# Kernel optimization log

Hardware: AMD Instinct MI355X
Metric: run time of the kernel (lower is better)

Reference implementation:

```python
import jax, jax.numpy as jnp
import numpy as np

B, D, O = 16384, 1024, 2048
MU, LAM = 0.9, 0.1


def setup_inputs() -> dict:
    key = jax.random.key(0)
    ks = jax.random.split(key, 16)
    stdv = float(1.0 / np.sqrt(D))
    u = lambda k, shape, s: jax.random.uniform(k, shape, jnp.float32, -s, s)
    return {
        "x": jax.random.normal(ks[0], (B, D), jnp.float32),
        "x_ctx": jax.random.normal(ks[1], (B, D), jnp.float32),
        "classifier": u(ks[2], (O, D), stdv),
        "none_tensor": u(ks[3], (1, D), stdv),
        "ctx_q_w": u(ks[4], (O, D), stdv),
        "ctx_q_b": u(ks[5], (O,), stdv),
        "word_g_w": u(ks[6], (1, D), stdv),
        "word_g_b": u(ks[7], (1,), stdv),
        "tcq_w1": u(ks[8], (D, D), stdv),
        "tcq_b1": u(ks[9], (D,), stdv),
        "tcq_w2": u(ks[10], (O, D), stdv),
        "tcq_b2": u(ks[11], (O,), stdv),
        "history_input": 0.1 * jax.random.normal(ks[12], (O - 1, D), jnp.float32),
        "history_count": jax.random.randint(ks[13], (O - 1,), 0, 10),
        "labels": jax.random.randint(ks[14], (B,), 0, O),
    }


def reference(x, x_ctx, classifier, none_tensor, ctx_q_w, ctx_q_b,
              word_g_w, word_g_b, tcq_w1, tcq_b1, tcq_w2, tcq_b2,
              history_input, history_count, labels):
    mu, lam = MU, LAM
    # ---- update_history (torch.no_grad), vectorized over classes via segment_sum ----
    xs = jax.lax.stop_gradient(x)
    sums = jax.ops.segment_sum(xs, labels, num_segments=O)               # [O, D]
    counts = jax.ops.segment_sum(jnp.ones((B,), jnp.float32), labels, num_segments=O)  # [O]
    has = counts[1:] > 0                                                  # classes 1..O-1
    cls_mean = sums[1:] / jnp.maximum(counts[1:], 1.0)[:, None]
    hist = jnp.where(has[:, None], mu * history_input + cls_mean, history_input)
    cnt = history_count + has.astype(history_count.dtype)
    # ---- generate_substitute (mu < 1 branch) ----
    denom = 1.0 - jnp.power(mu, jnp.maximum(cnt, 1).astype(jnp.float32))[:, None]
    v = hist * (1.0 - mu) / denom                                        # [O-1, D]
    r_sub = jnp.concatenate([none_tensor, v], axis=0)                    # [O, D]
    ctx_logits = x_ctx @ ctx_q_w.T + ctx_q_b                              # [B, O]
    att_logits = jax.nn.gelu(x @ tcq_w1.T + tcq_b1, approximate=False) @ tcq_w2.T + tcq_b2  # [B, O]
    # ---- gated combine + bilinear classifier (training=True path: w uses ctx_logits) ----
    g_word = jax.nn.sigmoid(x @ word_g_w.T + word_g_b)                    # [B, 1]
    w = g_word * jax.nn.sigmoid(ctx_logits)                               # [B, O]
    # logits = sum(((1-w)*x[:,None,:] + w*r_sub) * classifier, -1), collapsed algebraically
    logits = (1.0 - w) * (x @ classifier.T) + w * jnp.einsum('od,od->o', r_sub, classifier)[None, :]
    # ---- losses on labels >= 0 (mask-weighted means, jit-safe) ----
    mask = (labels >= 0).astype(jnp.float32)
    n = jnp.maximum(mask.sum(), 1.0)
    lsm = jax.nn.log_softmax(logits, axis=-1)
    nll = -jnp.take_along_axis(lsm, jnp.maximum(labels, 0)[:, None], axis=1)[:, 0]
    ce = (mask * nll).sum() / n
    mse_row = jnp.mean((ctx_logits - att_logits) ** 2, axis=-1)
    mse = (mask * mse_row).sum() / n
    return (ce + lam * mse, logits)
```

## Files before the change

kernel.cpp:

```cpp
#include <hip/hip_runtime.h>
#include <cstdint>
#include <cstddef>

#define DEV __device__ __forceinline__

typedef __attribute__((ext_vector_type(4))) float f32x4;
typedef __attribute__((ext_vector_type(8))) short bf16x8;
typedef unsigned short ushort_t;
typedef __attribute__((ext_vector_type(8))) unsigned short ushort8;

static constexpr int B_ = 16384, D_ = 1024, O_ = 2048;
static constexpr float LAM_ = 0.1f;

static constexpr size_t WS_XBF   = 0;
static constexpr size_t WS_XCBF  = WS_XBF   + (size_t)B_ * D_ * 2;
static constexpr size_t WS_HBF   = WS_XCBF  + (size_t)B_ * D_ * 2;
static constexpr size_t WS_CLSBF = WS_HBF   + (size_t)B_ * D_ * 2;
static constexpr size_t WS_CTWBF = WS_CLSBF + (size_t)O_ * D_ * 2;
static constexpr size_t WS_W2BF  = WS_CTWBF + (size_t)O_ * D_ * 2;
static constexpr size_t WS_W1BF  = WS_W2BF  + (size_t)O_ * D_ * 2;
static constexpr size_t WS_SMALL = WS_W1BF  + (size_t)D_ * D_ * 2;
static constexpr size_t SM_COUNTS = 0;
static constexpr size_t SM_TSUM   = 8192;
static constexpr size_t SM_MSE    = 16384;
static constexpr size_t SM_ZERO_BYTES = 82176;
static constexpr size_t SM_S      = 82176;
static constexpr size_t SM_GWORD  = 90368;
static constexpr size_t SM_CEROW  = 155904;

DEV float wave_sum(float v) {
  #pragma unroll
  for (int o = 32; o; o >>= 1) v += __shfl_xor(v, o, 64);
  return v;
}

DEV ushort_t f2bf1(float f) {
  union { float f; unsigned u; } c{f};
  unsigned r = c.u + 0x7fffu + ((c.u >> 16) & 1u);
  return (ushort_t)(r >> 16);
}

DEV float sigmoidf(float z) { return 1.0f / (1.0f + expf(-z)); }

DEV void gload_lds16(const ushort_t* g, ushort_t* l) {
  __builtin_amdgcn_global_load_lds((const __attribute__((address_space(1))) void*)g,
                                   (__attribute__((address_space(3))) void*)l, 16, 0, 0);
}

DEV void stage2(const ushort_t* __restrict__ s0, ushort_t* slot, int tid) {
  gload_lds16(s0, slot + tid * 8);
  gload_lds16(s0 + 128 * 1024, slot + (tid + 512) * 8);
}

DEV f32x4 mfma16(bf16x8 a, bf16x8 b, f32x4 c) {
  return __builtin_amdgcn_mfma_f32_16x16x32_bf16(a, b, c, 0, 0, 0);
}

#define DSR(dst, addr, off) \
  asm volatile("ds_read_b128 %0, %1 offset:" off : "=v"(dst) : "v"(addr))

template<int N> DEV void wait_vm() {
  if constexpr (N == 8)      asm volatile("s_waitcnt vmcnt(8)" ::: "memory");
  else if constexpr (N == 6) asm volatile("s_waitcnt vmcnt(6)" ::: "memory");
  else if constexpr (N == 4) asm volatile("s_waitcnt vmcnt(4)" ::: "memory");
  else if constexpr (N == 2) asm volatile("s_waitcnt vmcnt(2)" ::: "memory");
  else                       asm volatile("s_waitcnt vmcnt(0)" ::: "memory");
}

__global__ __launch_bounds__(256) void f2bf_kernel(const float* __restrict__ in,
                                                   ushort_t* __restrict__ out, int n8) {
  int i = blockIdx.x * 256 + threadIdx.x;
  if (i >= n8) return;
  const float4* p = (const float4*)(in + (size_t)i * 8);
  float4 a = p[0], b = p[1];
  ushort8 o;
  o[0] = f2bf1(a.x); o[1] = f2bf1(a.y); o[2] = f2bf1(a.z); o[3] = f2bf1(a.w);
  o[4] = f2bf1(b.x); o[5] = f2bf1(b.y); o[6] = f2bf1(b.z); o[7] = f2bf1(b.w);
  *(ushort8*)(out + (size_t)i * 8) = o;
}

__global__ __launch_bounds__(256) void rowdot_kernel(const float* __restrict__ x,
    const float* __restrict__ cls, const float* __restrict__ wg,
    const float* __restrict__ wgb, const int* __restrict__ labels,
    float* __restrict__ tsum, float* __restrict__ counts, float* __restrict__ g_word) {
  int wave = threadIdx.x >> 6, lane = threadIdx.x & 63;
  int row = blockIdx.x * 4 + wave;
  const float* xr = x + (size_t)row * D_;
  int lab = labels[row];
  const float* cr = cls + (size_t)max(lab, 0) * D_;
  float t = 0.f, g = 0.f;
  #pragma unroll
  for (int j = 0; j < 4; ++j) {
    int d = j * 256 + lane * 4;
    float4 xv = *(const float4*)(xr + d);
    float4 cv = *(const float4*)(cr + d);
    float4 wv = *(const float4*)(wg + d);
    t += xv.x * cv.x + xv.y * cv.y + xv.z * cv.z + xv.w * cv.w;
    g += xv.x * wv.x + xv.y * wv.y + xv.z * wv.z + xv.w * wv.w;
  }
  t = wave_sum(t); g = wave_sum(g);
  if (lane == 0) {
    if (lab >= 0) {
      atomicAdd(&tsum[lab], t);
      atomicAdd(&counts[lab], 1.0f);
    }
    g_word[row] = sigmoidf(g + wgb[0]);
  }
}

__global__ __launch_bounds__(256) void scls_kernel(const float* __restrict__ cls,
    const float* __restrict__ none_t, const float* __restrict__ hist,
    const int* __restrict__ hcnt, const float* __restrict__ counts,
    const float* __restrict__ tsum, float* __restrict__ s) {
  int wave = threadIdx.x >> 6, lane = threadIdx.x & 63;
  int o = blockIdx.x * 4 + wave;
  if (o >= O_) return;
  const float* cr = cls + (size_t)o * D_;
  const float* src = (o == 0) ? none_t : hist + (size_t)(o - 1) * D_;
  float dv = 0.f;
  #pragma unroll
  for (int j = 0; j < 4; ++j) {
    int d = j * 256 + lane * 4;
    float4 a = *(const float4*)(src + d);
    float4 c = *(const float4*)(cr + d);
    dv += a.x * c.x + a.y * c.y + a.z * c.z + a.w * c.w;
  }
  dv = wave_sum(dv);
  if (lane == 0) {
    if (o == 0) { s[0] = dv; }
    else {
      float co = counts[o];
      bool has = co > 0.f;
      int cnt = hcnt[o - 1] + (has ? 1 : 0);
      float denom = 1.f - powf(0.9f, (float)max(cnt, 1));
      float val = has ? (0.9f * dv + tsum[o] / fmaxf(co, 1.f)) : dv;
      s[o] = (0.1f / denom) * val;
    }
  }
}

template<bool S01, bool S23, int W0, int W1, int W2, int W3, bool RLAST>
DEV void tile4(int t, const ushort_t* __restrict__ sA0, const ushort_t* __restrict__ sB0,
               ushort_t* lds, int tid, unsigned aoffB, unsigned boffB,
               bf16x8 (&bA)[2][4], bf16x8 (&bB)[2][4], f32x4 (&acc)[8][4]) {
  const unsigned sl0 = (unsigned)(((2 * t) & 3) * 16384);
  const unsigned sl1 = (unsigned)(((2 * t + 1) & 3) * 16384);
  const unsigned sl2 = (unsigned)(((2 * t + 2) & 3) * 16384);
  const unsigned aA0 = aoffB + sl0;
  const unsigned aA1 = aoffB + sl1, aB1 = boffB + 65536u + sl1;
  const unsigned aA2 = aoffB + sl2, aB2 = boffB + 65536u + sl2;
  DSR(bA[1][0], aA0, "4096"); DSR(bA[1][1], aA0, "5120");
  DSR(bA[1][2], aA0, "6144"); DSR(bA[1][3], aA0, "7168");
  if constexpr (S01) stage2(sA0 + (size_t)(2 * t + 3) * 32, lds + ((2 * t + 3) & 3) * 8192, tid);
  asm volatile("s_waitcnt lgkmcnt(4)");
  __builtin_amdgcn_sched_barrier(0);
  __builtin_amdgcn_s_setprio(1);
  #pragma unroll
  for (int m = 0; m < 4; m++)
    #pragma unroll
    for (int n = 0; n < 4; n++) acc[m][n] = mfma16(bA[0][m], bB[0][n], acc[m][n]);
  __builtin_amdgcn_s_setprio(0);
  __builtin_amdgcn_sched_barrier(0);
  wait_vm<W0>();
  __builtin_amdgcn_s_barrier();
  DSR(bB[1][0], aB1, "0"); DSR(bB[1][1], aB1, "1024");
  DSR(bB[1][2], aB1, "2048"); DSR(bB[1][3], aB1, "3072");
  DSR(bA[0][0], aA1, "0"); DSR(bA[0][1], aA1, "1024");
  DSR(bA[0][2], aA1, "2048"); DSR(bA[0][3], aA1, "3072");
  if constexpr (S01) stage2(sB0 + (size_t)(2 * t + 3) * 32, lds + 32768 + ((2 * t + 3) & 3) * 8192, tid);
  asm volatile("s_waitcnt lgkmcnt(8)");
  __builtin_amdgcn_sched_barrier(0);
  __builtin_amdgcn_s_setprio(1);
  #pragma unroll
  for (int m = 0; m < 4; m++)
    #pragma unroll
    for (int n = 0; n < 4; n++) acc[m + 4][n] = mfma16(bA[1][m], bB[0][n], acc[m + 4][n]);
  __builtin_amdgcn_s_setprio(0);
  __builtin_amdgcn_sched_barrier(0);
  wait_vm<W1>();
  __builtin_amdgcn_s_barrier();
  DSR(bA[1][0], aA1, "4096"); DSR(bA[1][1], aA1, "5120");
  DSR(bA[1][2], aA1, "6144"); DSR(bA[1][3], aA1, "7168");
  if constexpr (S23) stage2(sA0 + (size_t)(2 * t + 4) * 32, lds + ((2 * t + 4) & 3) * 8192, tid);
  asm volatile("s_waitcnt lgkmcnt(4)");
  __builtin_amdgcn_sched_barrier(0);
  __builtin_amdgcn_s_setprio(1);
  #pragma unroll
  for (int m = 0; m < 4; m++)
    #pragma unroll
    for (int n = 0; n < 4; n++) acc[m][n] = mfma16(bA[0][m], bB[1][n], acc[m][n]);
  __builtin_amdgcn_s_setprio(0);
  __builtin_amdgcn_sched_barrier(0);
  wait_vm<W2>();
  __builtin_amdgcn_s_barrier();
  if constexpr (!RLAST) {
    DSR(bB[0][0], aB2, "0"); DSR(bB[0][1], aB2, "1024");
    DSR(bB[0][2], aB2, "2048"); DSR(bB[0][3], aB2, "3072");
    DSR(bA[0][0], aA2, "0"); DSR(bA[0][1], aA2, "1024");
    DSR(bA[0][2], aA2, "2048"); DSR(bA[0][3], aA2, "3072");
  }
  if constexpr (S23) stage2(sB0 + (size_t)(2 * t + 4) * 32, lds + 32768 + ((2 * t + 4) & 3) * 8192, tid);
  if constexpr (RLAST) asm volatile("s_waitcnt lgkmcnt(0)");
  else                 asm volatile("s_waitcnt lgkmcnt(8)");
  __builtin_amdgcn_sched_barrier(0);
  __builtin_amdgcn_s_setprio(1);
  #pragma unroll
  for (int m = 0; m < 4; m++)
    #pragma unroll
    for (int n = 0; n < 4; n++) acc[m + 4][n] = mfma16(bA[1][m], bB[1][n], acc[m + 4][n]);
  __builtin_amdgcn_s_setprio(0);
  __builtin_amdgcn_sched_barrier(0);
  wait_vm<W3>();
  __builtin_amdgcn_s_barrier();
}

template<int EPI, int NTSHIFT>
__global__ __launch_bounds__(512, 2) void gemm8_kernel(
    const ushort_t* __restrict__ A, const ushort_t* __restrict__ Bmat,
    const float* __restrict__ bias, float* __restrict__ fout,
    ushort_t* __restrict__ hout, const float* __restrict__ g_word,
    const float* __restrict__ svec, float* __restrict__ mse_row) {
  __shared__ __align__(16) ushort_t lds[65536];
  const int tid = threadIdx.x, lane = tid & 63, wave = tid >> 6;
  const int wr = wave >> 2, wc = wave & 3;
  const int nwg = 64 << NTSHIFT, cpx = nwg >> 3;
  int bid = blockIdx.x;
  int wg = (bid & 7) * cpx + (bid >> 3);
  const int bm = wg >> NTSHIFT, bn = wg & ((1 << NTSHIFT) - 1);
  const int NCOL = 256 << NTSHIFT;
  const int qsrc = (tid & 3) ^ ((tid >> 3) & 3);
  const ushort_t* sA0 = A + ((size_t)bm * 256 + (tid >> 2)) * 1024 + qsrc * 8;
  const ushort_t* sB0 = Bmat + ((size_t)bn * 256 + (tid >> 2)) * 1024 + qsrc * 8;
  const int qrd = (lane >> 4) ^ (((lane & 15) >> 1) & 3);
  const unsigned aoffB = (unsigned)(((wr * 128 + (lane & 15)) * 32 + qrd * 8) * 2);
  const unsigned boffB = (unsigned)(((wc * 64 + (lane & 15)) * 32 + qrd * 8) * 2);
  f32x4 acc[8][4] = {};
  stage2(sA0, lds, tid);
  stage2(sB0, lds + 32768, tid);
  stage2(sA0 + 32, lds + 8192, tid);
  stage2(sB0 + 32, lds + 32768 + 8192, tid);
  stage2(sA0 + 64, lds + 2 * 8192, tid);
  stage2(sB0 + 64, lds + 32768 + 2 * 8192, tid);
  asm volatile("s_waitcnt vmcnt(8)" ::: "memory");
  __builtin_amdgcn_s_barrier();
  bf16x8 bA[2][4], bB[2][4];
  {
    const unsigned aB0 = boffB + 65536u;
    DSR(bB[0][0], aB0, "0"); DSR(bB[0][1], aB0, "1024");
    DSR(bB[0][2], aB0, "2048"); DSR(bB[0][3], aB0, "3072");
    DSR(bA[0][0], aoffB, "0"); DSR(bA[0][1], aoffB, "1024");
    DSR(bA[0][2], aoffB, "2048"); DSR(bA[0][3], aoffB, "3072");
  }
  for (int t = 0; t < 14; ++t)
    tile4<true, true, 6, 6, 6, 6, false>(t, sA0, sB0, lds, tid, aoffB, boffB, bA, bB, acc);
  tile4<true, false, 6, 6, 4, 2, false>(14, sA0, sB0, lds, tid, aoffB, boffB, bA, bB, acc);
  tile4<false, false, 0, 0, 0, 0, true>(15, sA0, sB0, lds, tid, aoffB, boffB, bA, bB, acc);
  #pragma unroll
  for (int m = 0; m < 8; m++) {
    #pragma unroll
    for (int i = 0; i < 4; i++) {
      int row = bm * 256 + wr * 128 + m * 16 + (lane >> 4) * 4 + i;
      float gw = 0.f, msum = 0.f;
      if constexpr (EPI == 3) gw = g_word[row];
      #pragma unroll
      for (int n = 0; n < 4; n++) {
        int col = bn * 256 + wc * 64 + n * 16 + (lane & 15);
        float v = acc[m][n][i];
        if constexpr (EPI == 0) {
          float z = v + bias[col];
          float gl = 0.5f * z * (1.f + erff(z * 0.70710678118f));
          hout[(size_t)row * 1024 + col] = f2bf1(gl);
        } else if constexpr (EPI == 1) {
          fout[(size_t)row * NCOL + col] = v + bias[col];
        } else if constexpr (EPI == 2) {
          float att = v + bias[col];
          float ctx = fout[(size_t)row * NCOL + col];
          float d = ctx - att;
          msum += d * d;
        } else {
          size_t off = (size_t)row * NCOL + col;
          float ctx = fout[off];
          float w = gw * sigmoidf(ctx);
          fout[off] = (1.f - w) * v + w * svec[col];
        }
      }
      if constexpr (EPI == 2) {
        #pragma unroll
        for (int o = 1; o < 16; o <<= 1) msum += __shfl_xor(msum, o, 64);
        if ((lane & 15) == 0) atomicAdd(&mse_row[row], msum);
      }
    }
  }
}

__global__ __launch_bounds__(256) void ce_kernel(const float* __restrict__ logits,
    const int* __restrict__ labels, float* __restrict__ ce_row) {
  int row = blockIdx.x, t = threadIdx.x, lane = t & 63, wave = t >> 6;
  const float* lr = logits + (size_t)row * O_;
  float v[8];
  float m = -INFINITY;
  #pragma unroll
  for (int j = 0; j < 8; j++) { v[j] = lr[t + j * 256]; m = fmaxf(m, v[j]); }
  #pragma unroll
  for (int o = 32; o; o >>= 1) m = fmaxf(m, __shfl_xor(m, o, 64));
  __shared__ float red[8];
  if (lane == 0) red[wave] = m;
  __syncthreads();
  m = fmaxf(fmaxf(red[0], red[1]), fmaxf(red[2], red[3]));
  float se = 0.f;
  #pragma unroll
  for (int j = 0; j < 8; j++) se += expf(v[j] - m);
  se = wave_sum(se);
  if (lane == 0) red[4 + wave] = se;
  __syncthreads();
  if (t == 0) {
    float bs = red[4] + red[5] + red[6] + red[7];
    int lab = labels[row];
    float nll = 0.f;
    if (lab >= 0) nll = -(lr[lab] - m - logf(bs));
    ce_row[row] = nll;
  }
}

__global__ __launch_bounds__(256) void finalize_kernel(const float* __restrict__ ce_row,
    const float* __restrict__ mse_row, const int* __restrict__ labels,
    float* __restrict__ out0) {
  int t = threadIdx.x, lane = t & 63, wave = t >> 6;
  float sn = 0.f, sm = 0.f, sc = 0.f;
  for (int i = t; i < B_; i += 256) {
    if (labels[i] >= 0) { sn += ce_row[i]; sm += mse_row[i]; sc += 1.f; }
  }
  sn = wave_sum(sn); sm = wave_sum(sm); sc = wave_sum(sc);
  __shared__ float r0[4], r1[4], r2[4];
  if (lane == 0) { r0[wave] = sn; r1[wave] = sm; r2[wave] = sc; }
  __syncthreads();
  if (t == 0) {
    float a = r0[0] + r0[1] + r0[2] + r0[3];
    float b = r1[0] + r1[1] + r1[2] + r1[3];
    float c = r2[0] + r2[1] + r2[2] + r2[3];
    out0[0] = (a + LAM_ * (b / (float)O_)) / fmaxf(c, 1.f);
  }
}

extern "C" void kernel_launch(void* const* d_in, const int* in_sizes, int n_in,
                              void* d_out, int out_size, void* d_ws, size_t ws_size,
                              hipStream_t stream) {
  const float* x        = (const float*)d_in[0];
  const float* x_ctx    = (const float*)d_in[1];
  const float* cls      = (const float*)d_in[2];
  const float* none_t   = (const float*)d_in[3];
  const float* ctx_q_w  = (const float*)d_in[4];
  const float* ctx_q_b  = (const float*)d_in[5];
  const float* word_g_w = (const float*)d_in[6];
  const float* word_g_b = (const float*)d_in[7];
  const float* w1       = (const float*)d_in[8];
  const float* b1       = (const float*)d_in[9];
  const float* w2       = (const float*)d_in[10];
  const float* b2       = (const float*)d_in[11];
  const float* hist     = (const float*)d_in[12];
  const int*   hcnt     = (const int*)d_in[13];
  const int*   labels   = (const int*)d_in[14];

  float* out  = (float*)d_out;
  float* out1 = out + 1;
  char* ws = (char*)d_ws;

  ushort_t* xbf   = (ushort_t*)(ws + WS_XBF);
  ushort_t* xcbf  = (ushort_t*)(ws + WS_XCBF);
  ushort_t* hbf   = (ushort_t*)(ws + WS_HBF);
  ushort_t* clsbf = (ushort_t*)(ws + WS_CLSBF);
  ushort_t* ctwbf = (ushort_t*)(ws + WS_CTWBF);
  ushort_t* w2bf  = (ushort_t*)(ws + WS_W2BF);
  ushort_t* w1bf  = (ushort_t*)(ws + WS_W1BF);
  float* counts   = (float*)(ws + WS_SMALL + SM_COUNTS);
  float* tsum     = (float*)(ws + WS_SMALL + SM_TSUM);
  float* mse_row  = (float*)(ws + WS_SMALL + SM_MSE);
  float* s        = (float*)(ws + WS_SMALL + SM_S);
  float* g_word   = (float*)(ws + WS_SMALL + SM_GWORD);
  float* ce_row   = (float*)(ws + WS_SMALL + SM_CEROW);

  hipMemsetAsync(ws + WS_SMALL, 0, SM_ZERO_BYTES, stream);

  f2bf_kernel<<<8192, 256, 0, stream>>>(x, xbf, B_ * D_ / 8);
  f2bf_kernel<<<8192, 256, 0, stream>>>(x_ctx, xcbf, B_ * D_ / 8);
  f2bf_kernel<<<1024, 256, 0, stream>>>(cls, clsbf, O_ * D_ / 8);
  f2bf_kernel<<<1024, 256, 0, stream>>>(ctx_q_w, ctwbf, O_ * D_ / 8);
  f2bf_kernel<<<1024, 256, 0, stream>>>(w2, w2bf, O_ * D_ / 8);
  f2bf_kernel<<<512, 256, 0, stream>>>(w1, w1bf, D_ * D_ / 8);

  rowdot_kernel<<<B_ / 4, 256, 0, stream>>>(x, cls, word_g_w, word_g_b, labels,
                                            tsum, counts, g_word);
  scls_kernel<<<O_ / 4, 256, 0, stream>>>(cls, none_t, hist, hcnt, counts, tsum, s);

  gemm8_kernel<0, 2><<<64 * 4, 512, 0, stream>>>(xbf, w1bf, b1, nullptr, hbf,
                                                 nullptr, nullptr, nullptr);
  gemm8_kernel<1, 3><<<64 * 8, 512, 0, stream>>>(xcbf, ctwbf, ctx_q_b, out1, nullptr,
                                                 nullptr, nullptr, nullptr);
  gemm8_kernel<2, 3><<<64 * 8, 512, 0, stream>>>(hbf, w2bf, b2, out1, nullptr,
                                                 nullptr, nullptr, mse_row);
  gemm8_kernel<3, 3><<<64 * 8, 512, 0, stream>>>(xbf, clsbf, nullptr, out1, nullptr,
                                                 g_word, s, nullptr);

  ce_kernel<<<B_, 256, 0, stream>>>(out1, labels, ce_row);
  finalize_kernel<<<1, 256, 0, stream>>>(ce_row, mse_row, labels, out);
}
```

Measured before the change: 455.0 us.

## Add alternative GEMM main-loop schedules for the second and classifier GEMMs

Adds two alternative K-loop schedules for the bf16 GEMM kernel, selected by a new template parameter. One alternates half-tile LDS reads and MFMA bursts with extra barriers and full lgkmcnt waits. The other loads all eight A fragments per k-step and issues 32 MFMAs per phase. The tcq_w2 GEMM now uses the first and the classifier GEMM uses the second, in place of the software-pipelined double-buffered register schedule. This lowers register pressure and simplifies ordering, but it drops the overlap of LDS reads with MFMA and adds more barriers.

Result: no change. 461.9 us (+1.5%).

```diff
diff --git a/kernel.cpp b/kernel.cpp
--- a/kernel.cpp
+++ b/kernel.cpp
@@ -139,8 +139,9 @@
   }
 }
 
+
 template<bool S01, bool S23, int W0, int W1, int W2, int W3, bool RLAST>
-DEV void tile4(int t, const ushort_t* __restrict__ sA0, const ushort_t* __restrict__ sB0,
+DEV void tileA(int t, const ushort_t* __restrict__ sA0, const ushort_t* __restrict__ sB0,
                ushort_t* lds, int tid, unsigned aoffB, unsigned boffB,
                bf16x8 (&bA)[2][4], bf16x8 (&bB)[2][4], f32x4 (&acc)[8][4]) {
   const unsigned sl0 = (unsigned)(((2 * t) & 3) * 16384);
@@ -214,7 +215,115 @@
   __builtin_amdgcn_s_barrier();
 }
 
-template<int EPI, int NTSHIFT>
+template<bool S01, bool S23, int W1, int W3>
+DEV void tileB(int t, const ushort_t* __restrict__ sA0, const ushort_t* __restrict__ sB0,
+               ushort_t* lds, int tid, unsigned aoffB, unsigned boffB, f32x4 (&acc)[8][4]) {
+  const unsigned sl0 = (unsigned)(((2 * t) & 3) * 16384);
+  const unsigned sl1 = (unsigned)(((2 * t + 1) & 3) * 16384);
+  const unsigned aA0 = aoffB + sl0, aB0 = boffB + 65536u + sl0;
+  const unsigned aA1 = aoffB + sl1, aB1 = boffB + 65536u + sl1;
+  bf16x8 fA[4], fB[4];
+  DSR(fB[0], aB0, "0"); DSR(fB[1], aB0, "1024"); DSR(fB[2], aB0, "2048"); DSR(fB[3], aB0, "3072");
+  DSR(fA[0], aA0, "0"); DSR(fA[1], aA0, "1024"); DSR(fA[2], aA0, "2048"); DSR(fA[3], aA0, "3072");
+  if constexpr (S01) stage2(sA0 + (size_t)(2 * t + 3) * 32, lds + ((2 * t + 3) & 3) * 8192, tid);
+  __builtin_amdgcn_s_barrier();
+  asm volatile("s_waitcnt lgkmcnt(0)");
+  __builtin_amdgcn_sched_barrier(0);
+  __builtin_amdgcn_s_setprio(1);
+  #pragma unroll
+  for (int m = 0; m < 4; m++)
+    #pragma unroll
+    for (int n = 0; n < 4; n++) acc[m][n] = mfma16(fA[m], fB[n], acc[m][n]);
+  __builtin_amdgcn_s_setprio(0);
+  __builtin_amdgcn_s_barrier();
+  DSR(fA[0], aA0, "4096"); DSR(fA[1], aA0, "5120"); DSR(fA[2], aA0, "6144"); DSR(fA[3], aA0, "7168");
+  if constexpr (S01) stage2(sB0 + (size_t)(2 * t + 3) * 32, lds + 32768 + ((2 * t + 3) & 3) * 8192, tid);
+  __builtin_amdgcn_s_barrier();
+  asm volatile("s_waitcnt lgkmcnt(0)");
+  __builtin_amdgcn_sched_barrier(0);
+  __builtin_amdgcn_s_setprio(1);
+  #pragma unroll
+  for (int m = 0; m < 4; m++)
+    #pragma unroll
+    for (int n = 0; n < 4; n++) acc[m + 4][n] = mfma16(fA[m], fB[n], acc[m + 4][n]);
+  __builtin_amdgcn_s_setprio(0);
+  wait_vm<W1>();
+  __builtin_amdgcn_s_barrier();
+  DSR(fB[0], aB1, "0"); DSR(fB[1], aB1, "1024"); DSR(fB[2], aB1, "2048"); DSR(fB[3], aB1, "3072");
+  DSR(fA[0], aA1, "0"); DSR(fA[1], aA1, "1024"); DSR(fA[2], aA1, "2048"); DSR(fA[3], aA1, "3072");
+  if constexpr (S23) stage2(sA0 + (size_t)(2 * t + 4) * 32, lds + ((2 * t + 4) & 3) * 8192, tid);
+  __builtin_amdgcn_s_barrier();
+  asm volatile("s_waitcnt lgkmcnt(0)");
+  __builtin_amdgcn_sched_barrier(0);
+  __builtin_amdgcn_s_setprio(1);
+  #pragma unroll
+  for (int m = 0; m < 4; m++)
+    #pragma unroll
+    for (int n = 0; n < 4; n++) acc[m][n] = mfma16(fA[m], fB[n], acc[m][n]);
+  __builtin_amdgcn_s_setprio(0);
+  __builtin_amdgcn_s_barrier();
+  DSR(fA[0], aA1, "4096"); DSR(fA[1], aA1, "5120"); DSR(fA[2], aA1, "6144"); DSR(fA[3], aA1, "7168");
+  if constexpr (S23) stage2(sB0 + (size_t)(2 * t + 4) * 32, lds + 32768 + ((2 * t + 4) & 3) * 8192, tid);
+  __builtin_amdgcn_s_barrier();
+  asm volatile("s_waitcnt lgkmcnt(0)");
+  __builtin_amdgcn_sched_barrier(0);
+  __builtin_amdgcn_s_setprio(1);
+  #pragma unroll
+  for (int m = 0; m < 4; m++)
+    #pragma unroll
+    for (int n = 0; n < 4; n++) acc[m + 4][n] = mfma16(fA[m], fB[n], acc[m + 4][n]);
+  __builtin_amdgcn_s_setprio(0);
+  wait_vm<W3>();
+  __builtin_amdgcn_s_barrier();
+}
+
+template<bool S01, bool S23, int WA, int WB>
+DEV void tileC(int t, const ushort_t* __restrict__ sA0, const ushort_t* __restrict__ sB0,
+               ushort_t* lds, int tid, unsigned aoffB, unsigned boffB, f32x4 (&acc)[8][4]) {
+  const unsigned sl0 = (unsigned)(((2 * t) & 3) * 16384);
+  const unsigned sl1 = (unsigned)(((2 * t + 1) & 3) * 16384);
+  const unsigned aA0 = aoffB + sl0, aB0 = boffB + 65536u + sl0;
+  const unsigned aA1 = aoffB + sl1, aB1 = boffB + 65536u + sl1;
+  bf16x8 fA[8], fB[4];
+  DSR(fB[0], aB0, "0"); DSR(fB[1], aB0, "1024"); DSR(fB[2], aB0, "2048"); DSR(fB[3], aB0, "3072");
+  DSR(fA[0], aA0, "0"); DSR(fA[1], aA0, "1024"); DSR(fA[2], aA0, "2048"); DSR(fA[3], aA0, "3072");
+  DSR(fA[4], aA0, "4096"); DSR(fA[5], aA0, "5120"); DSR(fA[6], aA0, "6144"); DSR(fA[7], aA0, "7168");
+  if constexpr (S01) {
+    stage2(sA0 + (size_t)(2 * t + 3) * 32, lds + ((2 * t + 3) & 3) * 8192, tid);
+    stage2(sB0 + (size_t)(2 * t + 3) * 32, lds + 32768 + ((2 * t + 3) & 3) * 8192, tid);
+  }
+  __builtin_amdgcn_s_barrier();
+  asm volatile("s_waitcnt lgkmcnt(0)");
+  __builtin_amdgcn_sched_barrier(0);
+  __builtin_amdgcn_s_setprio(1);
+  #pragma unroll
+  for (int m = 0; m < 8; m++)
+    #pragma unroll
+    for (int n = 0; n < 4; n++) acc[m][n] = mfma16(fA[m], fB[n], acc[m][n]);
+  __builtin_amdgcn_s_setprio(0);
+  wait_vm<WA>();
+  __builtin_amdgcn_s_barrier();
+  DSR(fB[0], aB1, "0"); DSR(fB[1], aB1, "1024"); DSR(fB[2], aB1, "2048"); DSR(fB[3], aB1, "3072");
+  DSR(fA[0], aA1, "0"); DSR(fA[1], aA1, "1024"); DSR(fA[2], aA1, "2048"); DSR(fA[3], aA1, "3072");
+  DSR(fA[4], aA1, "4096"); DSR(fA[5], aA1, "5120"); DSR(fA[6], aA1, "6144"); DSR(fA[7], aA1, "7168");
+  if constexpr (S23) {
+    stage2(sA0 + (size_t)(2 * t + 4) * 32, lds + ((2 * t + 4) & 3) * 8192, tid);
+    stage2(sB0 + (size_t)(2 * t + 4) * 32, lds + 32768 + ((2 * t + 4) & 3) * 8192, tid);
+  }
+  __builtin_amdgcn_s_barrier();
+  asm volatile("s_waitcnt lgkmcnt(0)");
+  __builtin_amdgcn_sched_barrier(0);
+  __builtin_amdgcn_s_setprio(1);
+  #pragma unroll
+  for (int m = 0; m < 8; m++)
+    #pragma unroll
+    for (int n = 0; n < 4; n++) acc[m][n] = mfma16(fA[m], fB[n], acc[m][n]);
+  __builtin_amdgcn_s_setprio(0);
+  wait_vm<WB>();
+  __builtin_amdgcn_s_barrier();
+}
+
+template<int EPI, int NTSHIFT, int SCHED>
 __global__ __launch_bounds__(512, 2) void gemm8_kernel(
     const ushort_t* __restrict__ A, const ushort_t* __restrict__ Bmat,
     const float* __restrict__ bias, float* __restrict__ fout,
@@ -243,18 +352,30 @@
   stage2(sB0 + 64, lds + 32768 + 2 * 8192, tid);
   asm volatile("s_waitcnt vmcnt(8)" ::: "memory");
   __builtin_amdgcn_s_barrier();
-  bf16x8 bA[2][4], bB[2][4];
-  {
-    const unsigned aB0 = boffB + 65536u;
-    DSR(bB[0][0], aB0, "0"); DSR(bB[0][1], aB0, "1024");
-    DSR(bB[0][2], aB0, "2048"); DSR(bB[0][3], aB0, "3072");
-    DSR(bA[0][0], aoffB, "0"); DSR(bA[0][1], aoffB, "1024");
-    DSR(bA[0][2], aoffB, "2048"); DSR(bA[0][3], aoffB, "3072");
-  }
-  for (int t = 0; t < 14; ++t)
-    tile4<true, true, 6, 6, 6, 6, false>(t, sA0, sB0, lds, tid, aoffB, boffB, bA, bB, acc);
-  tile4<true, false, 6, 6, 4, 2, false>(14, sA0, sB0, lds, tid, aoffB, boffB, bA, bB, acc);
-  tile4<false, false, 0, 0, 0, 0, true>(15, sA0, sB0, lds, tid, aoffB, boffB, bA, bB, acc);
+  if constexpr (SCHED == 0) {
+    bf16x8 bA[2][4], bB[2][4];
+    {
+      const unsigned aB0 = boffB + 65536u;
+      DSR(bB[0][0], aB0, "0"); DSR(bB[0][1], aB0, "1024");
+      DSR(bB[0][2], aB0, "2048"); DSR(bB[0][3], aB0, "3072");
+      DSR(bA[0][0], aoffB, "0"); DSR(bA[0][1], aoffB, "1024");
+      DSR(bA[0][2], aoffB, "2048"); DSR(bA[0][3], aoffB, "3072");
+    }
+    for (int t = 0; t < 14; ++t)
+      tileA<true, true, 6, 6, 6, 6, false>(t, sA0, sB0, lds, tid, aoffB, boffB, bA, bB, acc);
+    tileA<true, false, 6, 6, 4, 2, false>(14, sA0, sB0, lds, tid, aoffB, boffB, bA, bB, acc);
+    tileA<false, false, 0, 0, 0, 0, true>(15, sA0, sB0, lds, tid, aoffB, boffB, bA, bB, acc);
+  } else if constexpr (SCHED == 1) {
+    for (int t = 0; t < 14; ++t)
+      tileB<true, true, 6, 6>(t, sA0, sB0, lds, tid, aoffB, boffB, acc);
+    tileB<true, false, 6, 4>(14, sA0, sB0, lds, tid, aoffB, boffB, acc);
+    tileB<false, false, 0, 0>(15, sA0, sB0, lds, tid, aoffB, boffB, acc);
+  } else {
+    for (int t = 0; t < 14; ++t)
+      tileC<true, true, 4, 4>(t, sA0, sB0, lds, tid, aoffB, boffB, acc);
+    tileC<true, false, 4, 4>(14, sA0, sB0, lds, tid, aoffB, boffB, acc);
+    tileC<false, false, 0, 0>(15, sA0, sB0, lds, tid, aoffB, boffB, acc);
+  }
   #pragma unroll
   for (int m = 0; m < 8; m++) {
     #pragma unroll
@@ -392,14 +513,14 @@
                                             tsum, counts, g_word);
   scls_kernel<<<O_ / 4, 256, 0, stream>>>(cls, none_t, hist, hcnt, counts, tsum, s);
 
-  gemm8_kernel<0, 2><<<64 * 4, 512, 0, stream>>>(xbf, w1bf, b1, nullptr, hbf,
-                                                 nullptr, nullptr, nullptr);
-  gemm8_kernel<1, 3><<<64 * 8, 512, 0, stream>>>(xcbf, ctwbf, ctx_q_b, out1, nullptr,
-                                                 nullptr, nullptr, nullptr);
-  gemm8_kernel<2, 3><<<64 * 8, 512, 0, stream>>>(hbf, w2bf, b2, out1, nullptr,
-                                                 nullptr, nullptr, mse_row);
-  gemm8_kernel<3, 3><<<64 * 8, 512, 0, stream>>>(xbf, clsbf, nullptr, out1, nullptr,
-                                                 g_word, s, nullptr);
+  gemm8_kernel<0, 2, 0><<<64 * 4, 512, 0, stream>>>(xbf, w1bf, b1, nullptr, hbf,
+                                                    nullptr, nullptr, nullptr);
+  gemm8_kernel<1, 3, 0><<<64 * 8, 512, 0, stream>>>(xcbf, ctwbf, ctx_q_b, out1, nullptr,
+                                                    nullptr, nullptr, nullptr);
+  gemm8_kernel<2, 3, 1><<<64 * 8, 512, 0, stream>>>(hbf, w2bf, b2, out1, nullptr,
+                                                    nullptr, nullptr, mse_row);
+  gemm8_kernel<3, 3, 2><<<64 * 8, 512, 0, stream>>>(xbf, clsbf, nullptr, out1, nullptr,
+                                                    g_word, s, nullptr);
 
   ce_kernel<<<B_, 256, 0, stream>>>(out1, labels, ce_row);
   finalize_kernel<<<1, 256, 0, stream>>>(ce_row, mse_row, labels, out);
```
